# Performance work log

Hardware: AMD Instinct MI355X
Metric: run time of the kernel (lower is better)

Reference implementation:

```python
import jax, jax.numpy as jnp
import numpy as np

D_MODEL = 1024
NUM_HEADS = 16
D_K = 1024
D_V = 1024
D_IN = 1024
THETA = 10000.0
B, S = 2, 2048


def setup_inputs() -> dict:
    key = jax.random.key(0)
    k1, k2, k3, k4, k5 = jax.random.split(key, 5)
    std_qkv = (2.0 / (D_IN + D_K)) ** 0.5
    std_o = (2.0 / (D_V + D_MODEL)) ** 0.5
    x = jax.random.normal(k1, (B, S, D_IN), jnp.float32)
    wq = jax.random.normal(k2, (D_IN, D_K), jnp.float32) * std_qkv
    wk = jax.random.normal(k3, (D_IN, D_K), jnp.float32) * std_qkv
    wv = jax.random.normal(k4, (D_IN, D_V), jnp.float32) * std_qkv
    wo = jax.random.normal(k5, (D_V, D_MODEL), jnp.float32) * std_o
    return {"x": x, "wq": wq, "wk": wk, "wv": wv, "wo": wo}


def _rope(t, theta):
    # t: (H, B, S, hd) -- interleaved-pair RoPE, angles pos * theta^(-2i/hd)
    hd = t.shape[-1]
    inv_freq = 1.0 / (theta ** (jnp.arange(0, hd, 2, dtype=jnp.float32) / hd))  # (hd/2,)
    pos = jnp.arange(t.shape[-2], dtype=jnp.float32)
    ang = pos[:, None] * inv_freq[None, :]                                       # (S, hd/2)
    cos, sin = jnp.cos(ang), jnp.sin(ang)
    tp = t.reshape(t.shape[:-1] + (hd // 2, 2))
    t0, t1 = tp[..., 0], tp[..., 1]
    out = jnp.stack([t0 * cos - t1 * sin, t0 * sin + t1 * cos], axis=-1)
    return out.reshape(t.shape)


def reference(x, wq, wk, wv, wo):
    b, s, _ = x.shape
    hd = D_K // NUM_HEADS
    hdv = D_V // NUM_HEADS
    # fused QKV proj (math identical to concat-then-matmul)
    q = jnp.einsum('bsd,de->bse', x, wq).reshape(b, s, NUM_HEADS, hd).transpose(2, 0, 1, 3)
    k = jnp.einsum('bsd,de->bse', x, wk).reshape(b, s, NUM_HEADS, hd).transpose(2, 0, 1, 3)
    v = jnp.einsum('bsd,de->bse', x, wv).reshape(b, s, NUM_HEADS, hdv).transpose(2, 0, 1, 3)
    q = _rope(q, THETA)
    k = _rope(k, THETA)
    scale = 1.0 / jnp.sqrt(jnp.asarray(hd, jnp.float32))
    scores = jnp.einsum('hbqd,hbkd->hbqk', q, k) * scale                 # (H,B,S,S)
    causal = jnp.tril(jnp.ones((s, s), dtype=bool))
    scores = jnp.where(causal, scores, -jnp.inf)
    attn = jax.nn.softmax(scores, axis=-1)
    o = jnp.einsum('hbqk,hbkd->hbqd', attn, v)                            # (H,B,S,hdv)
    o = o.transpose(1, 2, 0, 3).reshape(b, s, D_V)                        # merge heads (outer)
    return jnp.einsum('bsd,de->bse', o, wo)
```

## Files before the change

### kernel.cpp

```cpp
#include <hip/hip_runtime.h>
#include <stdint.h>

typedef __attribute__((ext_vector_type(8))) short short8;
typedef __attribute__((ext_vector_type(4))) float f32x4;
typedef __attribute__((ext_vector_type(4))) unsigned short ushort4v;
typedef __attribute__((ext_vector_type(2))) unsigned int uint2v;

static __device__ __forceinline__ unsigned short f2b(float f) {
  union { float f; unsigned int u; } v; v.f = f;
  unsigned int r = v.u + 0x7FFFu + ((v.u >> 16) & 1u);
  return (unsigned short)(r >> 16);
}

static __device__ __forceinline__ float exp2fast(float x) {
#if __has_builtin(__builtin_amdgcn_exp2f)
  return __builtin_amdgcn_exp2f(x);
#else
  return exp2f(x);
#endif
}

static __device__ __forceinline__ unsigned int cvtpk(float lo, float hi) {
  unsigned int r;
  asm("v_cvt_pk_bf16_f32 %0, %1, %2" : "=v"(r) : "v"(lo), "v"(hi));
  return r;
}

static __device__ __forceinline__ void gload16(const void* g, void* l) {
  __builtin_amdgcn_global_load_lds(
      (const __attribute__((address_space(1))) unsigned int*)g,
      (__attribute__((address_space(3))) unsigned int*)l, 16, 0, 0);
}


__global__ __launch_bounds__(256) void cast_x_kernel(const float* __restrict__ x,
                                                     unsigned short* __restrict__ xb) {
  int i = (blockIdx.x * 256 + threadIdx.x) * 4;
  float4 v = *(const float4*)(x + i);
  ushort4v o = { f2b(v.x), f2b(v.y), f2b(v.z), f2b(v.w) };
  *(ushort4v*)(xb + i) = o;
}

__global__ __launch_bounds__(256) void transpose_cast_kernel(
    const float* __restrict__ wq, const float* __restrict__ wk,
    const float* __restrict__ wv, const float* __restrict__ wo,
    unsigned short* __restrict__ wT) {
  const int z = blockIdx.z;
  const float* src = (z == 0) ? wq : (z == 1) ? wk : (z == 2) ? wv : wo;
  unsigned short* dst = wT + (size_t)z * 1048576;
  __shared__ float t[32][33];
  const int tid = threadIdx.x;
  const int tx = tid & 31, ty = tid >> 5;
  const int n0 = blockIdx.x * 32, k0 = blockIdx.y * 32;
#pragma unroll
  for (int i = 0; i < 4; ++i) {
    int r = ty + i * 8;
    t[r][tx] = src[(size_t)(k0 + r) * 1024 + n0 + tx];
  }
  __syncthreads();
#pragma unroll
  for (int i = 0; i < 4; ++i) {
    int r = ty + i * 8;
    dst[(size_t)(n0 + r) * 1024 + k0 + tx] = f2b(t[tx][r]);
  }
}

__global__ __launch_bounds__(256) void rope_tab_kernel(float* __restrict__ ct,
                                                       float* __restrict__ st) {
  int i = blockIdx.x * 256 + threadIdx.x;
  int s = i >> 5, p = i & 31;
  float ang = (float)s * powf(10000.0f, -(float)(2 * p) / 64.0f);
  ct[i] = cosf(ang);
  st[i] = sinf(ang);
}


__global__ __launch_bounds__(256) void gemm_kernel(
    const unsigned short* __restrict__ A, const unsigned short* __restrict__ WT,
    unsigned short* __restrict__ Qb, unsigned short* __restrict__ Kb,
    unsigned short* __restrict__ VTb, float* __restrict__ Fout,
    const float* __restrict__ ctab, const float* __restrict__ stab, int finalMode) {
  __shared__ unsigned short As[128 * 32];
  __shared__ unsigned short Bs[128 * 32];
  const int tid = threadIdx.x;
  const int w = tid >> 6, lane = tid & 63;
  const int m0 = blockIdx.x * 128, n0 = blockIdx.y * 128;
  int mode;
  const unsigned short* Bt;
  if (finalMode) { mode = 3; Bt = WT; }
  else { mode = blockIdx.z; Bt = WT + (size_t)mode * 1048576; }
  const int wr = w >> 1, wc = w & 1;
  const int srow = lane >> 2, scol = lane & 3;
  f32x4 acc[4][4] = {};
  for (int k0 = 0; k0 < 1024; k0 += 32) {
#pragma unroll
    for (int c = 0; c < 2; ++c) {
      int chunk = w * 2 + c;
      gload16(A + (size_t)(m0 + chunk * 16 + srow) * 1024 + k0 + scol * 8,
              (char*)As + chunk * 1024);
      gload16(Bt + (size_t)(n0 + chunk * 16 + srow) * 1024 + k0 + scol * 8,
              (char*)Bs + chunk * 1024);
    }
    __syncthreads();
    short8 af[4], bf[4];
#pragma unroll
    for (int i = 0; i < 4; ++i) {
      af[i] = *(const short8*)((const char*)As +
              ((wr * 64 + i * 16 + (lane & 15)) * 64 + (lane >> 4) * 16));
      bf[i] = *(const short8*)((const char*)Bs +
              ((wc * 64 + i * 16 + (lane & 15)) * 64 + (lane >> 4) * 16));
    }
#pragma unroll
    for (int i = 0; i < 4; ++i)
#pragma unroll
      for (int j = 0; j < 4; ++j)
        acc[i][j] = __builtin_amdgcn_mfma_f32_16x16x32_bf16(af[i], bf[j], acc[i][j], 0, 0, 0);
    __syncthreads();
  }

  if (mode < 2) {
    unsigned short* dst = mode ? Kb : Qb;
    const float qscale = mode ? 1.0f : 0.125f * 1.44269504088896f;
#pragma unroll
    for (int i = 0; i < 4; ++i) {
#pragma unroll
      for (int j = 0; j < 4; ++j) {
        int n = n0 + wc * 64 + j * 16 + (lane & 15);
        int h = n >> 6, d = n & 63;
        int pairIdx = d >> 1;
        bool even = (n & 1) == 0;
#pragma unroll
        for (int r = 0; r < 4; ++r) {
          int m = m0 + wr * 64 + i * 16 + (lane >> 4) * 4 + r;
          int b = m >> 11, s = m & 2047;
          float v = acc[i][j][r];
          float pv = __shfl_xor(v, 1);
          float c = ctab[s * 32 + pairIdx], sn = stab[s * 32 + pairIdx];
          float ov = (even ? (v * c - pv * sn) : (pv * sn + v * c)) * qscale;
          dst[(size_t)((h * 2 + b) * 2048 + s) * 64 + d] = f2b(ov);
        }
      }
    }
  } else if (mode == 2) {
#pragma unroll
    for (int i = 0; i < 4; ++i) {
#pragma unroll
      for (int j = 0; j < 4; ++j) {
        int n = n0 + wc * 64 + j * 16 + (lane & 15);
        int h = n >> 6, d = n & 63;
        int mBase = m0 + wr * 64 + i * 16 + (lane >> 4) * 4;
        int b = mBase >> 11, s = mBase & 2047;
        ushort4v pk = { f2b(acc[i][j][0]), f2b(acc[i][j][1]),
                        f2b(acc[i][j][2]), f2b(acc[i][j][3]) };
        *(ushort4v*)(VTb + (size_t)((h * 2 + b) * 64 + d) * 2048 + s) = pk;
      }
    }
  } else {
#pragma unroll
    for (int i = 0; i < 4; ++i)
#pragma unroll
      for (int j = 0; j < 4; ++j) {
        int n = n0 + wc * 64 + j * 16 + (lane & 15);
#pragma unroll
        for (int r = 0; r < 4; ++r) {
          int m = m0 + wr * 64 + i * 16 + (lane >> 4) * 4 + r;
          Fout[(size_t)m * 1024 + n] = acc[i][j][r];
        }
      }
  }
}


__device__ __forceinline__ void proc_tile(
    const short8 aq[2], const unsigned short* Ksb, const unsigned short* Vsb,
    char* Psw, int lq, int lh, int wq16, bool diag,
    float& m, float& l, f32x4* o) {
  const int swq = (lq & 7) << 4;
  f32x4 sacc[4] = {};
  __builtin_amdgcn_s_setprio(1);
#pragma unroll
  for (int ct = 0; ct < 4; ++ct) {
    const char* base = (const char*)Ksb + (ct * 16 + lq) * 128;
#pragma unroll
    for (int half = 0; half < 2; ++half) {
      short8 ak = *(const short8*)(base + ((half * 64 + lh * 16) ^ swq));
      sacc[ct] = __builtin_amdgcn_mfma_f32_16x16x32_bf16(ak, aq[half], sacc[ct], 0, 0, 0);
    }
  }
  __builtin_amdgcn_s_setprio(0);

  if (diag) {
    int rel = wq16 + lq - 4 * lh;
#pragma unroll
    for (int ct = 0; ct < 4; ++ct)
#pragma unroll
      for (int r = 0; r < 4; ++r)
        if (ct * 16 + r > rel) sacc[ct][r] = -__builtin_inff();
  }

  float mx0 = fmaxf(fmaxf(sacc[0][0], sacc[0][1]), fmaxf(sacc[0][2], sacc[0][3]));
  float mx1 = fmaxf(fmaxf(sacc[1][0], sacc[1][1]), fmaxf(sacc[1][2], sacc[1][3]));
  float mx2 = fmaxf(fmaxf(sacc[2][0], sacc[2][1]), fmaxf(sacc[2][2], sacc[2][3]));
  float mx3 = fmaxf(fmaxf(sacc[3][0], sacc[3][1]), fmaxf(sacc[3][2], sacc[3][3]));
  float mx = fmaxf(fmaxf(mx0, mx1), fmaxf(mx2, mx3));
  mx = fmaxf(mx, __shfl_xor(mx, 16));
  mx = fmaxf(mx, __shfl_xor(mx, 32));
  float nm = fmaxf(m, mx);
  float al = exp2fast(m - nm);
  m = nm;
  float ps = 0.f;
#pragma unroll
  for (int ct = 0; ct < 4; ++ct)
#pragma unroll
    for (int r = 0; r < 4; ++r) {
      float p = exp2fast(sacc[ct][r] - nm);
      sacc[ct][r] = p;
      ps += p;
    }
  ps += __shfl_xor(ps, 16);
  ps += __shfl_xor(ps, 32);
  l = l * al + ps;
#pragma unroll
  for (int ct = 0; ct < 4; ++ct)
#pragma unroll
    for (int r = 0; r < 4; ++r) o[ct][r] *= al;

#pragma unroll
  for (int ct = 0; ct < 4; ++ct) {
    uint2v pk = { cvtpk(sacc[ct][0], sacc[ct][1]), cvtpk(sacc[ct][2], sacc[ct][3]) };
    *(uint2v*)(Psw + lq * 128 + ((ct * 32 + lh * 8) ^ swq)) = pk;
  }
  __builtin_amdgcn_wave_barrier();
  short8 pa[2];
#pragma unroll
  for (int half = 0; half < 2; ++half)
    pa[half] = *(const short8*)(Psw + lq * 128 + ((half * 64 + lh * 16) ^ swq));

  __builtin_amdgcn_s_setprio(1);
#pragma unroll
  for (int ct = 0; ct < 4; ++ct) {
    const char* base = (const char*)Vsb + (ct * 16 + lq) * 128;
#pragma unroll
    for (int half = 0; half < 2; ++half) {
      short8 av = *(const short8*)(base + ((half * 64 + lh * 16) ^ swq));
      o[ct] = __builtin_amdgcn_mfma_f32_16x16x32_bf16(av, pa[half], o[ct], 0, 0, 0);
    }
  }
  __builtin_amdgcn_s_setprio(0);
}

__device__ __forceinline__ void store_o(
    const f32x4* o, float l, char* Psw, unsigned short* __restrict__ Ob,
    int lane, int lq, int lh, int w, int qb, int h, int b) {
  float invl = 1.0f / l;
#pragma unroll
  for (int ct = 0; ct < 4; ++ct)
#pragma unroll
    for (int r = 0; r < 4; ++r) {
      int d = ct * 16 + lh * 4 + r;
      *(unsigned short*)(Psw + lq * 128 + ((2 * d) ^ ((lq & 7) << 4))) =
          f2b(o[ct][r] * invl);
    }
  __syncthreads();
#pragma unroll
  for (int pass = 0; pass < 2; ++pass) {
    int q2 = pass * 8 + (lane >> 3), d0 = (lane & 7) * 8;
    short8 vrow = *(const short8*)(Psw + q2 * 128 + ((2 * d0) ^ ((q2 & 7) << 4)));
    int s = qb + w * 16 + q2;
    *(short8*)(Ob + ((size_t)(b * 2048 + s)) * 1024 + h * 64 + d0) = vrow;
  }
  __syncthreads();
}

__global__ __launch_bounds__(256) void attn_kernel(
    const unsigned short* __restrict__ Qb, const unsigned short* __restrict__ Kb,
    const unsigned short* __restrict__ VTb, unsigned short* __restrict__ Ob) {
  __shared__ unsigned short Ks[2][64 * 64];
  __shared__ unsigned short Vs[2][64 * 64];
  __shared__ unsigned short Ps[4 * 16 * 64];
  const int tid = threadIdx.x, w = tid >> 6, lane = tid & 63;
  const int qtL = blockIdx.x, qtH = 31 - blockIdx.x;
  const int hb = blockIdx.y;
  const int h = hb >> 1, b = hb & 1;
  const unsigned short* Qhb = Qb + (size_t)hb * 2048 * 64;
  const unsigned short* Khb = Kb + (size_t)hb * 2048 * 64;
  const unsigned short* Vhb = VTb + (size_t)hb * 64 * 2048;
  char* Psw = (char*)Ps + w * 2048;
  const int lq = lane & 15, lh = lane >> 4;
  const int wq16 = w * 16;

  short8 aqL[2], aqH[2];
  {
    int rowL = qtL * 64 + wq16 + lq;
    int rowH = qtH * 64 + wq16 + lq;
#pragma unroll
    for (int half = 0; half < 2; ++half) {
      aqL[half] = *(const short8*)(Qhb + (size_t)rowL * 64 + half * 32 + lh * 8);
      aqH[half] = *(const short8*)(Qhb + (size_t)rowH * 64 + half * 32 + lh * 8);
    }
  }
  float mL = -__builtin_inff(), lL = 0.f;
  float mH = -__builtin_inff(), lH = 0.f;
  f32x4 oL[4] = {}, oH[4] = {};

  const int r0 = tid >> 3, f0 = tid & 7;
  const int so0 = r0 * 128 + ((f0 * 16) ^ ((r0 & 7) << 4));
  short8 gK[2], gV[2];
  gK[0] = *(const short8*)(Khb + (size_t)r0 * 64 + f0 * 8);
  gK[1] = *(const short8*)(Khb + (size_t)(r0 + 32) * 64 + f0 * 8);
  gV[0] = *(const short8*)(Vhb + (size_t)r0 * 2048 + f0 * 8);
  gV[1] = *(const short8*)(Vhb + (size_t)(r0 + 32) * 2048 + f0 * 8);
  *(short8*)((char*)Ks[0] + so0) = gK[0];
  *(short8*)((char*)Ks[0] + so0 + 32 * 128) = gK[1];
  *(short8*)((char*)Vs[0] + so0) = gV[0];
  *(short8*)((char*)Vs[0] + so0 + 32 * 128) = gV[1];
  __syncthreads();

  for (int kt = 0; kt <= qtH; ++kt) {
    const int cur = kt & 1;
    if (kt < qtH) {
      int kk0 = (kt + 1) * 64;
      gK[0] = *(const short8*)(Khb + (size_t)(kk0 + r0) * 64 + f0 * 8);
      gK[1] = *(const short8*)(Khb + (size_t)(kk0 + r0 + 32) * 64 + f0 * 8);
      gV[0] = *(const short8*)(Vhb + (size_t)r0 * 2048 + kk0 + f0 * 8);
      gV[1] = *(const short8*)(Vhb + (size_t)(r0 + 32) * 2048 + kk0 + f0 * 8);
    }
    proc_tile(aqH, Ks[cur], Vs[cur], Psw, lq, lh, wq16, kt == qtH, mH, lH, oH);
    if (kt <= qtL)
      proc_tile(aqL, Ks[cur], Vs[cur], Psw, lq, lh, wq16, kt == qtL, mL, lL, oL);
    if (kt < qtH) {
      *(short8*)((char*)Ks[cur ^ 1] + so0) = gK[0];
      *(short8*)((char*)Ks[cur ^ 1] + so0 + 32 * 128) = gK[1];
      *(short8*)((char*)Vs[cur ^ 1] + so0) = gV[0];
      *(short8*)((char*)Vs[cur ^ 1] + so0 + 32 * 128) = gV[1];
    }
    __syncthreads();
  }

  store_o(oL, lL, Psw, Ob, lane, lq, lh, w, qtL * 64, h, b);
  store_o(oH, lH, Psw, Ob, lane, lq, lh, w, qtH * 64, h, b);
}


extern "C" void kernel_launch(void* const* d_in, const int* in_sizes, int n_in,
                              void* d_out, int out_size, void* d_ws, size_t ws_size,
                              hipStream_t stream) {
  const float* x  = (const float*)d_in[0];
  const float* wq = (const float*)d_in[1];
  const float* wk = (const float*)d_in[2];
  const float* wv = (const float*)d_in[3];
  const float* wo = (const float*)d_in[4];
  float* out = (float*)d_out;

  char* ws = (char*)d_ws;
  const size_t SZ = 8388608;
  unsigned short* xb  = (unsigned short*)(ws);
  unsigned short* wT  = (unsigned short*)(ws + SZ);
  unsigned short* Qb  = (unsigned short*)(ws + 2 * SZ);
  unsigned short* Kb  = (unsigned short*)(ws + 3 * SZ);
  unsigned short* VTb = (unsigned short*)(ws + 4 * SZ);
  unsigned short* Ob  = (unsigned short*)(ws + 5 * SZ);
  float* ctab = (float*)(ws + 6 * SZ);
  float* stab = (float*)(ws + 6 * SZ + 262144);
  if (ws_size < 6 * SZ + 2 * 262144) return;

  cast_x_kernel<<<4096, 256, 0, stream>>>(x, xb);
  transpose_cast_kernel<<<dim3(32, 32, 4), 256, 0, stream>>>(wq, wk, wv, wo, wT);
  rope_tab_kernel<<<256, 256, 0, stream>>>(ctab, stab);
  gemm_kernel<<<dim3(32, 8, 3), 256, 0, stream>>>(xb, wT, Qb, Kb, VTb, nullptr, ctab, stab, 0);
  attn_kernel<<<dim3(16, 32), 256, 0, stream>>>(Qb, Kb, VTb, Ob);
  gemm_kernel<<<dim3(32, 8, 1), 256, 0, stream>>>(Ob, wT + 3 * 1048576, Qb, Kb, VTb, out,
                                                  ctab, stab, 1);
}
```

Measured before the change: 136.3 us.

## Share K/V fragments across paired query tiles and defer row-sum reduction

Restructures the attention inner loop so the low and high query tiles load K and V fragments from LDS once and issue their MFMAs together. The two tiles write P to separate LDS buffers, so their softmax work can interleave. The cross-lane row-sum shuffles move out of the per-tile loop and run once at the end, and max reductions use permlane swaps when available. The final output store drops its block-wide syncs in favour of per-wave handling. In exchange, register pressure and LDS use go up, which may lower occupancy.

Measured after the change: 165.3 us. +21.3%, slower.

```diff
diff --git a/kernel.cpp b/kernel.cpp
--- a/kernel.cpp
+++ b/kernel.cpp
@@ -24,6 +24,43 @@
   unsigned int r;
   asm("v_cvt_pk_bf16_f32 %0, %1, %2" : "=v"(r) : "v"(lo), "v"(hi));
   return r;
+}
+
+static __device__ __forceinline__ float xor16max(float x) {
+#if __has_builtin(__builtin_amdgcn_permlane16_swap)
+  unsigned u = __float_as_uint(x);
+  uint2v r = __builtin_amdgcn_permlane16_swap(u, u, false, false);
+  return fmaxf(__uint_as_float(r[0]), __uint_as_float(r[1]));
+#else
+  return fmaxf(x, __shfl_xor(x, 16));
+#endif
+}
+static __device__ __forceinline__ float xor32max(float x) {
+#if __has_builtin(__builtin_amdgcn_permlane32_swap)
+  unsigned u = __float_as_uint(x);
+  uint2v r = __builtin_amdgcn_permlane32_swap(u, u, false, false);
+  return fmaxf(__uint_as_float(r[0]), __uint_as_float(r[1]));
+#else
+  return fmaxf(x, __shfl_xor(x, 32));
+#endif
+}
+static __device__ __forceinline__ float xor16add(float x) {
+#if __has_builtin(__builtin_amdgcn_permlane16_swap)
+  unsigned u = __float_as_uint(x);
+  uint2v r = __builtin_amdgcn_permlane16_swap(u, u, false, false);
+  return __uint_as_float(r[0]) + __uint_as_float(r[1]);
+#else
+  return x + __shfl_xor(x, 16);
+#endif
+}
+static __device__ __forceinline__ float xor32add(float x) {
+#if __has_builtin(__builtin_amdgcn_permlane32_swap)
+  unsigned u = __float_as_uint(x);
+  uint2v r = __builtin_amdgcn_permlane32_swap(u, u, false, false);
+  return __uint_as_float(r[0]) + __uint_as_float(r[1]);
+#else
+  return x + __shfl_xor(x, 32);
+#endif
 }
 
 static __device__ __forceinline__ void gload16(const void* g, void* l) {
@@ -171,40 +208,37 @@
 }
 
 
-__device__ __forceinline__ void proc_tile(
-    const short8 aq[2], const unsigned short* Ksb, const unsigned short* Vsb,
-    char* Psw, int lq, int lh, int wq16, bool diag,
-    float& m, float& l, f32x4* o) {
+__device__ __forceinline__ short8 ldfrag(const unsigned short* base_, int ct, int half,
+                                         int lq, int lh) {
   const int swq = (lq & 7) << 4;
-  f32x4 sacc[4] = {};
-  __builtin_amdgcn_s_setprio(1);
+  return *(const short8*)((const char*)base_ + (ct * 16 + lq) * 128 +
+                          ((half * 64 + lh * 16) ^ swq));
+}
+
+__device__ __forceinline__ void qk8(f32x4* s, const short8* kf, const short8* aq) {
 #pragma unroll
   for (int ct = 0; ct < 4; ++ct) {
-    const char* base = (const char*)Ksb + (ct * 16 + lq) * 128;
-#pragma unroll
-    for (int half = 0; half < 2; ++half) {
-      short8 ak = *(const short8*)(base + ((half * 64 + lh * 16) ^ swq));
-      sacc[ct] = __builtin_amdgcn_mfma_f32_16x16x32_bf16(ak, aq[half], sacc[ct], 0, 0, 0);
-    }
-  }
-  __builtin_amdgcn_s_setprio(0);
-
-  if (diag) {
-    int rel = wq16 + lq - 4 * lh;
-#pragma unroll
-    for (int ct = 0; ct < 4; ++ct)
-#pragma unroll
-      for (int r = 0; r < 4; ++r)
-        if (ct * 16 + r > rel) sacc[ct][r] = -__builtin_inff();
-  }
-
-  float mx0 = fmaxf(fmaxf(sacc[0][0], sacc[0][1]), fmaxf(sacc[0][2], sacc[0][3]));
-  float mx1 = fmaxf(fmaxf(sacc[1][0], sacc[1][1]), fmaxf(sacc[1][2], sacc[1][3]));
-  float mx2 = fmaxf(fmaxf(sacc[2][0], sacc[2][1]), fmaxf(sacc[2][2], sacc[2][3]));
-  float mx3 = fmaxf(fmaxf(sacc[3][0], sacc[3][1]), fmaxf(sacc[3][2], sacc[3][3]));
+    s[ct] = __builtin_amdgcn_mfma_f32_16x16x32_bf16(kf[ct * 2], aq[0], s[ct], 0, 0, 0);
+    s[ct] = __builtin_amdgcn_mfma_f32_16x16x32_bf16(kf[ct * 2 + 1], aq[1], s[ct], 0, 0, 0);
+  }
+}
+
+__device__ __forceinline__ void cmask(f32x4* s, int rel) {
+#pragma unroll
+  for (int ct = 0; ct < 4; ++ct)
+#pragma unroll
+    for (int r = 0; r < 4; ++r)
+      if (ct * 16 + r > rel) s[ct][r] = -__builtin_inff();
+}
+
+__device__ __forceinline__ void softmax_path(f32x4* s, float& m, float& ls, f32x4* o) {
+  float mx0 = fmaxf(fmaxf(s[0][0], s[0][1]), fmaxf(s[0][2], s[0][3]));
+  float mx1 = fmaxf(fmaxf(s[1][0], s[1][1]), fmaxf(s[1][2], s[1][3]));
+  float mx2 = fmaxf(fmaxf(s[2][0], s[2][1]), fmaxf(s[2][2], s[2][3]));
+  float mx3 = fmaxf(fmaxf(s[3][0], s[3][1]), fmaxf(s[3][2], s[3][3]));
   float mx = fmaxf(fmaxf(mx0, mx1), fmaxf(mx2, mx3));
-  mx = fmaxf(mx, __shfl_xor(mx, 16));
-  mx = fmaxf(mx, __shfl_xor(mx, 32));
+  mx = xor16max(mx);
+  mx = xor32max(mx);
   float nm = fmaxf(m, mx);
   float al = exp2fast(m - nm);
   m = nm;
@@ -213,63 +247,46 @@
   for (int ct = 0; ct < 4; ++ct)
 #pragma unroll
     for (int r = 0; r < 4; ++r) {
-      float p = exp2fast(sacc[ct][r] - nm);
-      sacc[ct][r] = p;
+      float p = exp2fast(s[ct][r] - nm);
+      s[ct][r] = p;
       ps += p;
     }
-  ps += __shfl_xor(ps, 16);
-  ps += __shfl_xor(ps, 32);
-  l = l * al + ps;
+  ls = ls * al + ps;
 #pragma unroll
   for (int ct = 0; ct < 4; ++ct)
 #pragma unroll
     for (int r = 0; r < 4; ++r) o[ct][r] *= al;
-
+}
+
+__device__ __forceinline__ void pwrite(const f32x4* s, char* Psw, int lq, int lh) {
+  const int swq = (lq & 7) << 4;
 #pragma unroll
   for (int ct = 0; ct < 4; ++ct) {
-    uint2v pk = { cvtpk(sacc[ct][0], sacc[ct][1]), cvtpk(sacc[ct][2], sacc[ct][3]) };
+    uint2v pk = { cvtpk(s[ct][0], s[ct][1]), cvtpk(s[ct][2], s[ct][3]) };
     *(uint2v*)(Psw + lq * 128 + ((ct * 32 + lh * 8) ^ swq)) = pk;
   }
-  __builtin_amdgcn_wave_barrier();
-  short8 pa[2];
+}
+
+__device__ __forceinline__ void pread(short8* pa, const char* Psw, int lq, int lh) {
+  const int swq = (lq & 7) << 4;
 #pragma unroll
   for (int half = 0; half < 2; ++half)
     pa[half] = *(const short8*)(Psw + lq * 128 + ((half * 64 + lh * 16) ^ swq));
-
-  __builtin_amdgcn_s_setprio(1);
-#pragma unroll
-  for (int ct = 0; ct < 4; ++ct) {
-    const char* base = (const char*)Vsb + (ct * 16 + lq) * 128;
-#pragma unroll
-    for (int half = 0; half < 2; ++half) {
-      short8 av = *(const short8*)(base + ((half * 64 + lh * 16) ^ swq));
-      o[ct] = __builtin_amdgcn_mfma_f32_16x16x32_bf16(av, pa[half], o[ct], 0, 0, 0);
-    }
-  }
-  __builtin_amdgcn_s_setprio(0);
-}
-
-__device__ __forceinline__ void store_o(
-    const f32x4* o, float l, char* Psw, unsigned short* __restrict__ Ob,
-    int lane, int lq, int lh, int w, int qb, int h, int b) {
+}
+
+__device__ __forceinline__ void store_path(
+    const f32x4* o, float ls, char* Psw, unsigned short* __restrict__ Ob,
+    int lq, int lh, int qrow_base, int h, int b) {
+  float l = xor32add(xor16add(ls));
   float invl = 1.0f / l;
+  const int swq = (lq & 7) << 4;
 #pragma unroll
   for (int ct = 0; ct < 4; ++ct)
 #pragma unroll
     for (int r = 0; r < 4; ++r) {
       int d = ct * 16 + lh * 4 + r;
-      *(unsigned short*)(Psw + lq * 128 + ((2 * d) ^ ((lq & 7) << 4))) =
-          f2b(o[ct][r] * invl);
-    }
-  __syncthreads();
-#pragma unroll
-  for (int pass = 0; pass < 2; ++pass) {
-    int q2 = pass * 8 + (lane >> 3), d0 = (lane & 7) * 8;
-    short8 vrow = *(const short8*)(Psw + q2 * 128 + ((2 * d0) ^ ((q2 & 7) << 4)));
-    int s = qb + w * 16 + q2;
-    *(short8*)(Ob + ((size_t)(b * 2048 + s)) * 1024 + h * 64 + d0) = vrow;
-  }
-  __syncthreads();
+      *(unsigned short*)(Psw + lq * 128 + ((2 * d) ^ swq)) = f2b(o[ct][r] * invl);
+    }
 }
 
 __global__ __launch_bounds__(256) void attn_kernel(
@@ -277,7 +294,7 @@
     const unsigned short* __restrict__ VTb, unsigned short* __restrict__ Ob) {
   __shared__ unsigned short Ks[2][64 * 64];
   __shared__ unsigned short Vs[2][64 * 64];
-  __shared__ unsigned short Ps[4 * 16 * 64];
+  __shared__ unsigned short Ps[2][4 * 16 * 64];
   const int tid = threadIdx.x, w = tid >> 6, lane = tid & 63;
   const int qtL = blockIdx.x, qtH = 31 - blockIdx.x;
   const int hb = blockIdx.y;
@@ -285,9 +302,11 @@
   const unsigned short* Qhb = Qb + (size_t)hb * 2048 * 64;
   const unsigned short* Khb = Kb + (size_t)hb * 2048 * 64;
   const unsigned short* Vhb = VTb + (size_t)hb * 64 * 2048;
-  char* Psw = (char*)Ps + w * 2048;
+  char* PsH = (char*)Ps[0] + w * 2048;
+  char* PsL = (char*)Ps[1] + w * 2048;
   const int lq = lane & 15, lh = lane >> 4;
   const int wq16 = w * 16;
+  const int rel = wq16 + lq - 4 * lh;
 
   short8 aqL[2], aqH[2];
   {
@@ -299,8 +318,8 @@
       aqH[half] = *(const short8*)(Qhb + (size_t)rowH * 64 + half * 32 + lh * 8);
     }
   }
-  float mL = -__builtin_inff(), lL = 0.f;
-  float mH = -__builtin_inff(), lH = 0.f;
+  float mL = -__builtin_inff(), lsL = 0.f;
+  float mH = -__builtin_inff(), lsH = 0.f;
   f32x4 oL[4] = {}, oH[4] = {};
 
   const int r0 = tid >> 3, f0 = tid & 7;
@@ -325,9 +344,65 @@
       gV[0] = *(const short8*)(Vhb + (size_t)r0 * 2048 + kk0 + f0 * 8);
       gV[1] = *(const short8*)(Vhb + (size_t)(r0 + 32) * 2048 + kk0 + f0 * 8);
     }
-    proc_tile(aqH, Ks[cur], Vs[cur], Psw, lq, lh, wq16, kt == qtH, mH, lH, oH);
-    if (kt <= qtL)
-      proc_tile(aqL, Ks[cur], Vs[cur], Psw, lq, lh, wq16, kt == qtL, mL, lL, oL);
+    if (kt <= qtL) {
+      short8 kf[8];
+#pragma unroll
+      for (int ct = 0; ct < 4; ++ct) {
+        kf[ct * 2] = ldfrag(Ks[cur], ct, 0, lq, lh);
+        kf[ct * 2 + 1] = ldfrag(Ks[cur], ct, 1, lq, lh);
+      }
+      f32x4 sH[4] = {}, sL[4] = {};
+      __builtin_amdgcn_s_setprio(1);
+      qk8(sH, kf, aqH);
+      qk8(sL, kf, aqL);
+      __builtin_amdgcn_s_setprio(0);
+      if (kt == qtL) cmask(sL, rel);
+      softmax_path(sH, mH, lsH, oH);
+      softmax_path(sL, mL, lsL, oL);
+      pwrite(sH, PsH, lq, lh);
+      pwrite(sL, PsL, lq, lh);
+      __builtin_amdgcn_wave_barrier();
+      short8 paH[2], paL[2];
+      pread(paH, PsH, lq, lh);
+      pread(paL, PsL, lq, lh);
+      __builtin_amdgcn_s_setprio(1);
+#pragma unroll
+      for (int ct = 0; ct < 4; ++ct) {
+        short8 v0 = ldfrag(Vs[cur], ct, 0, lq, lh);
+        short8 v1 = ldfrag(Vs[cur], ct, 1, lq, lh);
+        oH[ct] = __builtin_amdgcn_mfma_f32_16x16x32_bf16(v0, paH[0], oH[ct], 0, 0, 0);
+        oH[ct] = __builtin_amdgcn_mfma_f32_16x16x32_bf16(v1, paH[1], oH[ct], 0, 0, 0);
+        oL[ct] = __builtin_amdgcn_mfma_f32_16x16x32_bf16(v0, paL[0], oL[ct], 0, 0, 0);
+        oL[ct] = __builtin_amdgcn_mfma_f32_16x16x32_bf16(v1, paL[1], oL[ct], 0, 0, 0);
+      }
+      __builtin_amdgcn_s_setprio(0);
+    } else {
+      short8 kf[8];
+#pragma unroll
+      for (int ct = 0; ct < 4; ++ct) {
+        kf[ct * 2] = ldfrag(Ks[cur], ct, 0, lq, lh);
+        kf[ct * 2 + 1] = ldfrag(Ks[cur], ct, 1, lq, lh);
+      }
+      f32x4 sH[4] = {};
+      __builtin_amdgcn_s_setprio(1);
+      qk8(sH, kf, aqH);
+      __builtin_amdgcn_s_setprio(0);
+      if (kt == qtH) cmask(sH, rel);
+      softmax_path(sH, mH, lsH, oH);
+      pwrite(sH, PsH, lq, lh);
+      __builtin_amdgcn_wave_barrier();
+      short8 paH[2];
+      pread(paH, PsH, lq, lh);
+      __builtin_amdgcn_s_setprio(1);
+#pragma unroll
+      for (int ct = 0; ct < 4; ++ct) {
+        short8 v0 = ldfrag(Vs[cur], ct, 0, lq, lh);
+        short8 v1 = ldfrag(Vs[cur], ct, 1, lq, lh);
+        oH[ct] = __builtin_amdgcn_mfma_f32_16x16x32_bf16(v0, paH[0], oH[ct], 0, 0, 0);
+        oH[ct] = __builtin_amdgcn_mfma_f32_16x16x32_bf16(v1, paH[1], oH[ct], 0, 0, 0);
+      }
+      __builtin_amdgcn_s_setprio(0);
+    }
     if (kt < qtH) {
       *(short8*)((char*)Ks[cur ^ 1] + so0) = gK[0];
       *(short8*)((char*)Ks[cur ^ 1] + so0 + 32 * 128) = gK[1];
@@ -337,8 +412,20 @@
     __syncthreads();
   }
 
-  store_o(oL, lL, Psw, Ob, lane, lq, lh, w, qtL * 64, h, b);
-  store_o(oH, lH, Psw, Ob, lane, lq, lh, w, qtH * 64, h, b);
+  store_path(oH, lsH, PsH, Ob, lq, lh, qtH * 64 + wq16, h, b);
+  store_path(oL, lsL, PsL, Ob, lq, lh, qtL * 64 + wq16, h, b);
+  __builtin_amdgcn_wave_barrier();
+#pragma unroll
+  for (int pass = 0; pass < 2; ++pass) {
+    int q2 = pass * 8 + (lane >> 3), d0 = (lane & 7) * 8;
+    int swq2 = (q2 & 7) << 4;
+    short8 vH = *(const short8*)(PsH + q2 * 128 + ((2 * d0) ^ swq2));
+    short8 vL = *(const short8*)(PsL + q2 * 128 + ((2 * d0) ^ swq2));
+    int sH_ = qtH * 64 + wq16 + q2;
+    int sL_ = qtL * 64 + wq16 + q2;
+    *(short8*)(Ob + ((size_t)(b * 2048 + sH_)) * 1024 + h * 64 + d0) = vH;
+    *(short8*)(Ob + ((size_t)(b * 2048 + sL_)) * 1024 + h * 64 + d0) = vL;
+  }
 }
 
 
```
